# Performance work log

Hardware: AMD Instinct MI355X
Metric: run time of the kernel (lower is better)

## Reference

```python
import jax, jax.numpy as jnp
import numpy as np

N = 50000      # nodes
E = 800000     # edges (before self-loops)
IN_DIM = 256
HID = 128
HEADS = 4
HEAD_D = HID // HEADS
LAYERS = 2
EPS = 1e-5
SLOPE = 0.2    # GATv2 leaky_relu negative slope (PyG default)


def setup_inputs() -> dict:
    key = jax.random.key(0)
    ks = jax.random.split(key, 8)
    x = jax.random.normal(ks[0], (N, IN_DIM), dtype=jnp.float32)
    edge_index = jax.random.randint(ks[1], (2, E), 0, N, dtype=jnp.int64)
    s_in = (2.0 / (IN_DIM + HID)) ** 0.5
    s_h = (2.0 / (HID + HID)) ** 0.5
    return {
        'x': x,
        'W_in': jax.random.normal(ks[2], (IN_DIM, HID), dtype=jnp.float32) * s_in,
        'b_in': jnp.zeros((HID,), jnp.float32),
        'ln_in_g': jnp.ones((HID,), jnp.float32),
        'ln_in_b': jnp.zeros((HID,), jnp.float32),
        'Wl': jax.random.normal(ks[3], (LAYERS, HID, HID), dtype=jnp.float32) * s_h,
        'Wr': jax.random.normal(ks[4], (LAYERS, HID, HID), dtype=jnp.float32) * s_h,
        'att': jax.random.normal(ks[5], (LAYERS, HEADS, HEAD_D), dtype=jnp.float32) * s_h,
        'ln_g': jnp.ones((LAYERS, HID), jnp.float32),
        'ln_b': jnp.zeros((LAYERS, HID), jnp.float32),
        'edge_index': edge_index,
    }


def layer_norm(h, g, b):
    mu = jnp.mean(h, axis=-1, keepdims=True)
    var = jnp.mean(jnp.square(h - mu), axis=-1, keepdims=True)
    return (h - mu) * jax.lax.rsqrt(var + EPS) * g + b


def gatv2_conv(h, src, dst, Wl, Wr, att):
    # h: [N, HID]; src/dst: [E'] (self-loops included)
    xl = (h @ Wl).reshape(N, HEADS, HEAD_D)   # source transform (also message)
    xr = (h @ Wr).reshape(N, HEADS, HEAD_D)   # target transform
    e = jax.nn.leaky_relu(xl[src] + xr[dst], SLOPE)          # [E', H, D]
    logits = jnp.einsum('ehd,hd->eh', e, att)                # [E', H]
    # segment softmax over incoming edges of each dst node
    m = jax.lax.stop_gradient(jax.ops.segment_max(logits, dst, num_segments=N))
    a = jnp.exp(logits - m[dst])
    z = jax.ops.segment_sum(a, dst, num_segments=N)
    alpha = a / z[dst]                                       # [E', H]
    out = jax.ops.segment_sum(xl[src] * alpha[:, :, None], dst, num_segments=N)
    return out.reshape(N, HID)


def reference(x, W_in, b_in, ln_in_g, ln_in_b, Wl, Wr, att, ln_g, ln_b, edge_index):
    loops = jnp.arange(N, dtype=edge_index.dtype)
    src = jnp.concatenate([edge_index[0], loops])
    dst = jnp.concatenate([edge_index[1], loops])
    h = jax.nn.relu(layer_norm(x @ W_in + b_in, ln_in_g, ln_in_b))
    for l in range(LAYERS):
        h_new = jax.nn.elu(layer_norm(gatv2_conv(h, src, dst, Wl[l], Wr[l], att[l]), ln_g[l], ln_b[l]))
        h = h + h_new
    return h
```

## Files before the change

kernel.cpp:

```cpp
#include <hip/hip_runtime.h>
#include <hip/hip_bf16.h>


#define NN 50000
#define EE 800000
#define EP (EE + NN)
#define IN_DIM 256
#define HID 128
#define SLOPE 0.2f
#define LN_EPS 1e-5f
#define NB 196
#define L2E 1.4426950408889634f

typedef short s8v __attribute__((ext_vector_type(8)));
typedef float f4v __attribute__((ext_vector_type(4)));

__device__ __forceinline__ float u2f(unsigned int u) {
    union { unsigned int i; float f; } c; c.i = u; return c.f;
}
__device__ __forceinline__ unsigned short f2bf(float f) {
    union { float f; unsigned int i; } c; c.f = f;
    unsigned int r = (c.i + 0x7fffu + ((c.i >> 16) & 1u)) >> 16;
    return (unsigned short)r;
}
__device__ __forceinline__ void unpack8(const uint4 raw, float* m) {
    m[0] = u2f(raw.x << 16); m[1] = u2f(raw.x & 0xffff0000u);
    m[2] = u2f(raw.y << 16); m[3] = u2f(raw.y & 0xffff0000u);
    m[4] = u2f(raw.z << 16); m[5] = u2f(raw.z & 0xffff0000u);
    m[6] = u2f(raw.w << 16); m[7] = u2f(raw.w & 0xffff0000u);
}
__device__ __forceinline__ float quad_sum(float v) {
    v += __int_as_float(__builtin_amdgcn_update_dpp(
            0, __float_as_int(v), 0xB1 , 0xF, 0xF, true));
    v += __int_as_float(__builtin_amdgcn_update_dpp(
            0, __float_as_int(v), 0x4E , 0xF, 0xF, true));
    return v;
}

__global__ void prep_weights(const float* __restrict__ Win,
                             const float* __restrict__ Wl,
                             const float* __restrict__ Wr,
                             float4* __restrict__ wp) {
    const int sid = blockIdx.x * 256 + threadIdx.x;
    const float* W;
    int slot;
    if (sid < 4096) { W = Win; slot = sid; }
    else {
        const int m = (sid - 4096) >> 11;
        slot = (sid - 4096) & 2047;
        W = (m == 0) ? Wl : (m == 1) ? Wr : (m == 2) ? (Wl + 16384) : (Wr + 16384);
    }
    const int n = slot & 127;
    const int kbase = (slot >> 9) * 32 + ((slot >> 7) & 3) * 8;
    unsigned short o[8];
#pragma unroll
    for (int j = 0; j < 8; j++) o[j] = f2bf(W[(size_t)(kbase + j) * 128 + n]);
    wp[sid] = *(const float4*)o;
}

__global__ __launch_bounds__(256) void gemm_in_mfma(
        const float* __restrict__ x,
        const float4* __restrict__ wp,
        const float* __restrict__ bin,
        const float* __restrict__ g,
        const float* __restrict__ bb,
        unsigned short* __restrict__ hb) {
    __shared__ s8v wlds[4096];
    const int tid = threadIdx.x;
    const int wv = tid >> 6, lane = tid & 63;
    const int l15 = lane & 15, kseg = lane >> 4;
    const int row0 = blockIdx.x * 64 + wv * 16;
    const int arow = row0 + l15;
    const int r = (arow < NN) ? arow : 0;

    s8v afrag[8];
#pragma unroll
    for (int ks = 0; ks < 8; ks++) {
        const float* ap = x + (size_t)r * IN_DIM + ks * 32 + kseg * 8;
        const float4 a0 = *(const float4*)ap;
        const float4 a1 = *(const float4*)(ap + 4);
        unsigned short t[8] = { f2bf(a0.x), f2bf(a0.y), f2bf(a0.z), f2bf(a0.w),
                                f2bf(a1.x), f2bf(a1.y), f2bf(a1.z), f2bf(a1.w) };
        afrag[ks] = *(const s8v*)t;
    }

#pragma unroll
    for (int i = 0; i < 16; i++) {
        const int idx = i * 256 + tid;
        ((float4*)wlds)[idx] = wp[idx];
    }
    __syncthreads();

    f4v acc[8];
#pragma unroll
    for (int nb = 0; nb < 8; nb++) acc[nb] = (f4v){0.f, 0.f, 0.f, 0.f};
#pragma unroll
    for (int ks = 0; ks < 8; ks++) {
#pragma unroll
        for (int nb = 0; nb < 8; nb++) {
            const s8v bfrag = wlds[(ks * 4 + kseg) * 128 + nb * 16 + l15];
            acc[nb] = __builtin_amdgcn_mfma_f32_16x16x32_bf16(afrag[ks], bfrag, acc[nb], 0, 0, 0);
        }
    }

    float binv[8], gv[8], bbv[8];
#pragma unroll
    for (int nb = 0; nb < 8; nb++) {
        const int col = nb * 16 + l15;
        binv[nb] = bin[col]; gv[nb] = g[col]; bbv[nb] = bb[col];
    }
    float s1[4] = {0.f, 0.f, 0.f, 0.f}, s2[4] = {0.f, 0.f, 0.f, 0.f};
#pragma unroll
    for (int nb = 0; nb < 8; nb++)
#pragma unroll
        for (int reg = 0; reg < 4; reg++) {
            const float t = acc[nb][reg] + binv[nb];
            acc[nb][reg] = t;
            s1[reg] += t; s2[reg] += t * t;
        }
#pragma unroll
    for (int off = 1; off < 16; off <<= 1)
#pragma unroll
        for (int reg = 0; reg < 4; reg++) {
            s1[reg] += __shfl_xor(s1[reg], off);
            s2[reg] += __shfl_xor(s2[reg], off);
        }
    float mu[4], rstd[4];
#pragma unroll
    for (int reg = 0; reg < 4; reg++) {
        mu[reg] = s1[reg] / (float)HID;
        rstd[reg] = rsqrtf(s2[reg] / (float)HID - mu[reg] * mu[reg] + LN_EPS);
    }
    const int rbase = row0 + 4 * kseg;
#pragma unroll
    for (int reg = 0; reg < 4; reg++) {
        const int grow = rbase + reg;
        if (grow >= NN) continue;
#pragma unroll
        for (int nb = 0; nb < 8; nb++) {
            const int col = nb * 16 + l15;
            float v = (acc[nb][reg] - mu[reg]) * rstd[reg] * gv[nb] + bbv[nb];
            hb[(size_t)grow * HID + col] = f2bf(fmaxf(v, 0.f));
        }
    }
}

__global__ __launch_bounds__(256) void gemm_xlxr_mfma(
        const unsigned short* __restrict__ hb,
        const float4* __restrict__ wp,
        unsigned short* __restrict__ xl,
        unsigned short* __restrict__ xrb) {
    __shared__ s8v wlds[4096];
    const int tid = threadIdx.x;
    const int wv = tid >> 6, lane = tid & 63;
    const int l15 = lane & 15, kseg = lane >> 4;
    const int row0 = blockIdx.x * 64 + wv * 16;
    const int arow = row0 + l15;
    const int r = (arow < NN) ? arow : 0;

    s8v afrag[4];
#pragma unroll
    for (int ks = 0; ks < 4; ks++)
        afrag[ks] = *(const s8v*)(hb + (size_t)r * HID + ks * 32 + kseg * 8);

#pragma unroll
    for (int i = 0; i < 16; i++) {
        const int idx = i * 256 + tid;
        ((float4*)wlds)[idx] = wp[idx];
    }
    __syncthreads();

    f4v accL[8], accR[8];
#pragma unroll
    for (int nb = 0; nb < 8; nb++) {
        accL[nb] = (f4v){0.f, 0.f, 0.f, 0.f};
        accR[nb] = (f4v){0.f, 0.f, 0.f, 0.f};
    }
#pragma unroll
    for (int ks = 0; ks < 4; ks++) {
#pragma unroll
        for (int nb = 0; nb < 8; nb++) {
            const s8v bL = wlds[(ks * 4 + kseg) * 128 + nb * 16 + l15];
            accL[nb] = __builtin_amdgcn_mfma_f32_16x16x32_bf16(afrag[ks], bL, accL[nb], 0, 0, 0);
            const s8v bR = wlds[2048 + (ks * 4 + kseg) * 128 + nb * 16 + l15];
            accR[nb] = __builtin_amdgcn_mfma_f32_16x16x32_bf16(afrag[ks], bR, accR[nb], 0, 0, 0);
        }
    }

    const int rbase = row0 + 4 * kseg;
#pragma unroll
    for (int reg = 0; reg < 4; reg++) {
        const int grow = rbase + reg;
        if (grow >= NN) continue;
#pragma unroll
        for (int nb = 0; nb < 8; nb++) {
            const int col = nb * 16 + l15;
            xl[(size_t)grow * HID + col]  = f2bf(accL[nb][reg]);
            xrb[(size_t)grow * HID + col] = f2bf(accR[nb][reg]);
        }
    }
}

__global__ void dst_hist(const int* __restrict__ ei, int* __restrict__ cnt,
                         unsigned short* __restrict__ epos) {
    const long e = (long)blockIdx.x * 256 + threadIdx.x;
    if (e >= EP) return;
    const int d = (e < EE) ? ei[EE + e] : (int)(e - EE);
    epos[e] = (unsigned short)atomicAdd(&cnt[d], 1);
}

__global__ void scan_bsum(const int* __restrict__ cnt, int* __restrict__ bsum) {
    const int tid = threadIdx.x;
    const int i = blockIdx.x * 256 + tid;
    int v = (i < NN) ? cnt[i] : 0;
#pragma unroll
    for (int off = 1; off < 64; off <<= 1) v += __shfl_xor(v, off);
    __shared__ int ws[4];
    if ((tid & 63) == 0) ws[tid >> 6] = v;
    __syncthreads();
    if (tid == 0) bsum[blockIdx.x] = ws[0] + ws[1] + ws[2] + ws[3];
}

__global__ void scan_bpre(const int* __restrict__ bsum, int* __restrict__ bpre) {
    const int t = threadIdx.x;
    const int lane = t & 63, wv = t >> 6;
    const int v = (t < NB) ? bsum[t] : 0;
    int s = v;
#pragma unroll
    for (int off = 1; off < 64; off <<= 1) {
        const int u = __shfl_up(s, off);
        if (lane >= off) s += u;
    }
    __shared__ int wt[4];
    if (lane == 63) wt[wv] = s;
    __syncthreads();
    int add = 0;
    for (int w = 0; w < wv; w++) add += wt[w];
    if (t < NB) bpre[t] = s + add - v;
}

__global__ void scan_rowptr(const int* __restrict__ cnt,
                            const int* __restrict__ bpre,
                            int* __restrict__ rowptr) {
    const int tid = threadIdx.x;
    const int lane = tid & 63, wv = tid >> 6;
    const int i = blockIdx.x * 256 + tid;
    const int v = (i < NN) ? cnt[i] : 0;
    int s = v;
#pragma unroll
    for (int off = 1; off < 64; off <<= 1) {
        const int u = __shfl_up(s, off);
        if (lane >= off) s += u;
    }
    __shared__ int wt[4];
    if (lane == 63) wt[wv] = s;
    __syncthreads();
    int add = bpre[blockIdx.x];
    for (int w = 0; w < wv; w++) add += wt[w];
    const int excl = s + add - v;
    if (i < NN) rowptr[i] = excl;
    if (i == NN - 1) rowptr[NN] = excl + v;
}

__global__ void csr_scatter(const int* __restrict__ ei,
                            const int* __restrict__ rowptr,
                            const unsigned short* __restrict__ epos,
                            unsigned short* __restrict__ esrc16) {
    const long e = (long)blockIdx.x * 256 + threadIdx.x;
    if (e >= EP) return;
    int s, d;
    if (e < EE) { s = ei[e]; d = ei[EE + e]; }
    else        { s = d = (int)(e - EE); }
    esrc16[rowptr[d] + epos[e]] = (unsigned short)s;
}

__global__ __launch_bounds__(256) void gat_ln(
        const unsigned short* __restrict__ xl,
        const unsigned short* __restrict__ xrb,
        const float* __restrict__ att,
        const int* __restrict__ rowptr,
        const unsigned short* __restrict__ esrc16,
        const float* __restrict__ g,
        const float* __restrict__ b,
        const unsigned short* __restrict__ hres,
        float* __restrict__ dest,
        unsigned short* __restrict__ destb) {
    const int tid = threadIdx.x;
    const int lane = tid & 63;
    const int wv = tid >> 6;
    const int l16 = lane & 15;
    const int grp = lane >> 4;
    const int node = blockIdx.x * 16 + wv * 4 + grp;
    const int f0 = l16 * 8;

    float xrv[8], a06[8], a04[8];
    {
        const uint4 xraw = *(const uint4*)(xrb + (size_t)node * HID + f0);
        unpack8(xraw, xrv);
        const float4 t0 = *(const float4*)(att + f0);
        const float4 t1 = *(const float4*)(att + f0 + 4);
        float av[8] = { t0.x, t0.y, t0.z, t0.w, t1.x, t1.y, t1.z, t1.w };
#pragma unroll
        for (int j = 0; j < 8; j++) {
            a06[j] = 0.6f * L2E * av[j];
            a04[j] = 0.4f * L2E * av[j];
        }
    }
    const int beg = rowptr[node];
    const int deg = rowptr[node + 1] - beg;
    int dmax = deg;
    dmax = max(dmax, __shfl_xor(dmax, 16));
    dmax = max(dmax, __shfl_xor(dmax, 32));

    const char* xlbase = (const char*)xl + f0 * 2;
    const int gb = lane & 48;

    float acc[8];
#pragma unroll
    for (int j = 0; j < 8; j++) acc[j] = 0.f;
    float z = 0.f;

    int sb = (l16 < deg) ? (int)esrc16[beg + l16] : 0;

#define PROCR(RAW, VALID) do {                                              \
        float m[8];                                                         \
        unpack8((RAW), m);                                                  \
        float v = 0.f;                                                      \
        _Pragma("unroll")                                                   \
        for (int j = 0; j < 8; j++) {                                       \
            const float tt = m[j] + xrv[j];                                 \
            v += tt * a06[j] + fabsf(tt) * a04[j];                          \
        }                                                                   \
        v = quad_sum(v);                           \
        const float a = (VALID) ? __builtin_amdgcn_exp2f(v) : 0.f;          \
        z += a;                                                             \
        _Pragma("unroll")                                                   \
        for (int j = 0; j < 8; j++) acc[j] = fmaf(a, m[j], acc[j]);         \
    } while (0)

    for (int t = 0; t < dmax; t += 8) {
        if ((t & 15) == 0 && t) {
            sb = (t + l16 < deg) ? (int)esrc16[beg + t + l16] : 0;
        }
        int o[8];
#pragma unroll
        for (int i = 0; i < 8; i++)
            o[i] = __shfl(sb, gb | ((t + i) & 15)) << 8;
        uint4 r[8];
#pragma unroll
        for (int i = 0; i < 8; i++)
            r[i] = *(const uint4*)(xlbase + o[i]);
#pragma unroll
        for (int i = 0; i < 8; i++)
            PROCR(r[i], t + i < deg);
    }
#undef PROCR

    const float inv = 1.f / z;
    float o[8];
    float s1 = 0.f, s2 = 0.f;
#pragma unroll
    for (int j = 0; j < 8; j++) {
        o[j] = acc[j] * inv;
        s1 += o[j];
        s2 = fmaf(o[j], o[j], s2);
    }
#pragma unroll
    for (int off = 1; off < 16; off <<= 1) {
        s1 += __shfl_xor(s1, off);
        s2 += __shfl_xor(s2, off);
    }
    const float mu = s1 / (float)HID;
    const float rstd = rsqrtf(s2 / (float)HID - mu * mu + LN_EPS);

    float gv[8], bv[8], hv[8];
    {
        const float4 g0 = *(const float4*)(g + f0);
        const float4 g1 = *(const float4*)(g + f0 + 4);
        gv[0]=g0.x; gv[1]=g0.y; gv[2]=g0.z; gv[3]=g0.w;
        gv[4]=g1.x; gv[5]=g1.y; gv[6]=g1.z; gv[7]=g1.w;
        const float4 b0 = *(const float4*)(b + f0);
        const float4 b1 = *(const float4*)(b + f0 + 4);
        bv[0]=b0.x; bv[1]=b0.y; bv[2]=b0.z; bv[3]=b0.w;
        bv[4]=b1.x; bv[5]=b1.y; bv[6]=b1.z; bv[7]=b1.w;
        const uint4 hraw = *(const uint4*)(hres + (size_t)node * HID + f0);
        unpack8(hraw, hv);
    }
    float res[8];
#pragma unroll
    for (int j = 0; j < 8; j++) {
        float n = (o[j] - mu) * rstd * gv[j] + bv[j];
        n = (n > 0.f) ? n : (__builtin_amdgcn_exp2f(n * L2E) - 1.f);
        res[j] = hv[j] + n;
    }
    if (dest) {
        float* dp = dest + (size_t)node * HID + f0;
        *(float4*)dp       = (float4){res[0], res[1], res[2], res[3]};
        *(float4*)(dp + 4) = (float4){res[4], res[5], res[6], res[7]};
    }
    if (destb) {
        unsigned short o16[8];
#pragma unroll
        for (int j = 0; j < 8; j++) o16[j] = f2bf(res[j]);
        *(uint4*)(destb + (size_t)node * HID + f0) = *(const uint4*)o16;
    }
}

extern "C" void kernel_launch(void* const* d_in, const int* in_sizes, int n_in,
                              void* d_out, int out_size, void* d_ws, size_t ws_size,
                              hipStream_t stream) {
    const float* x       = (const float*)d_in[0];
    const float* W_in    = (const float*)d_in[1];
    const float* b_in    = (const float*)d_in[2];
    const float* ln_in_g = (const float*)d_in[3];
    const float* ln_in_b = (const float*)d_in[4];
    const float* Wl      = (const float*)d_in[5];
    const float* Wr      = (const float*)d_in[6];
    const float* att     = (const float*)d_in[7];
    const float* ln_g    = (const float*)d_in[8];
    const float* ln_b    = (const float*)d_in[9];
    const int*   ei      = (const int*)d_in[10];
    float* out = (float*)d_out;

    unsigned short* hb  = (unsigned short*)d_ws;
    unsigned short* hb2 = hb  + (size_t)NN * HID;
    unsigned short* xlb = hb2 + (size_t)NN * HID;
    unsigned short* xrb = xlb + (size_t)NN * HID;
    float4* wp = (float4*)(xrb + (size_t)NN * HID);
    int* cnt    = (int*)(wp + 12288);
    int* rowptr = cnt + NN;
    int* bsum   = rowptr + (NN + 1);
    int* bpre   = bsum + NB;
    unsigned short* epos   = (unsigned short*)(bpre + NB);
    unsigned short* esrc16 = epos + EP;

    prep_weights<<<48, 256, 0, stream>>>(W_in, Wl, Wr, wp);

    (void)hipMemsetAsync(cnt, 0, NN * sizeof(int), stream);
    const int eblocks = (EP + 255) / 256;
    dst_hist<<<eblocks, 256, 0, stream>>>(ei, cnt, epos);
    scan_bsum<<<NB, 256, 0, stream>>>(cnt, bsum);
    scan_bpre<<<1, 256, 0, stream>>>(bsum, bpre);
    scan_rowptr<<<NB, 256, 0, stream>>>(cnt, bpre, rowptr);
    csr_scatter<<<eblocks, 256, 0, stream>>>(ei, rowptr, epos, esrc16);

    const int mblocks = (NN + 63) / 64;
    gemm_in_mfma<<<mblocks, 256, 0, stream>>>(x, wp, b_in, ln_in_g, ln_in_b, hb);

    for (int l = 0; l < 2; l++) {
        const unsigned short* hsrc = (l == 0) ? hb : hb2;
        gemm_xlxr_mfma<<<mblocks, 256, 0, stream>>>(hsrc, wp + 4096 + l * 4096, xlb, xrb);
        gat_ln<<<NN / 16, 256, 0, stream>>>(xlb, xrb, att + (size_t)l * HID,
                                            rowptr, esrc16,
                                            ln_g + (size_t)l * HID,
                                            ln_b + (size_t)l * HID,
                                            hsrc,
                                            (l == 1) ? out : (float*)nullptr,
                                            (l == 0) ? hb2 : (unsigned short*)nullptr);
    }
}
```

Before: 189.3 us.

## Assign one wavefront per node, splitting edges across four lane groups

The GAT aggregation kernel now maps one 64-lane wavefront to each destination node instead of packing four nodes per wavefront. The four 16-lane groups each process a different edge, with partial accumulators and softmax denominators combined by cross-group shuffles, and only group 0 writes the LayerNorm result. This is meant to remove the load imbalance of padding each wavefront to the largest degree among its four nodes. The cost is fewer independent loads in flight per lane (one gather per iteration instead of eight batched), extra reduction shuffles, and four times as many blocks.

```diff
diff --git a/kernel.cpp b/kernel.cpp
--- a/kernel.cpp
+++ b/kernel.cpp
@@ -290,7 +290,7 @@
     const int wv = tid >> 6;
     const int l16 = lane & 15;
     const int grp = lane >> 4;
-    const int node = blockIdx.x * 16 + wv * 4 + grp;
+    const int node = blockIdx.x * 4 + wv;
     const int f0 = l16 * 8;
 
     float xrv[8], a06[8], a04[8];
@@ -308,19 +308,15 @@
     }
     const int beg = rowptr[node];
     const int deg = rowptr[node + 1] - beg;
-    int dmax = deg;
-    dmax = max(dmax, __shfl_xor(dmax, 16));
-    dmax = max(dmax, __shfl_xor(dmax, 32));
 
     const char* xlbase = (const char*)xl + f0 * 2;
-    const int gb = lane & 48;
 
     float acc[8];
 #pragma unroll
     for (int j = 0; j < 8; j++) acc[j] = 0.f;
     float z = 0.f;
 
-    int sb = (l16 < deg) ? (int)esrc16[beg + l16] : 0;
+    int sb = (lane < deg) ? (int)esrc16[beg + lane] : 0;
 
 #define PROCR(RAW, VALID) do {                                              \
         float m[8];                                                         \
@@ -338,23 +334,24 @@
         for (int j = 0; j < 8; j++) acc[j] = fmaf(a, m[j], acc[j]);         \
     } while (0)
 
-    for (int t = 0; t < dmax; t += 8) {
-        if ((t & 15) == 0 && t) {
-            sb = (t + l16 < deg) ? (int)esrc16[beg + t + l16] : 0;
-        }
-        int o[8];
-#pragma unroll
-        for (int i = 0; i < 8; i++)
-            o[i] = __shfl(sb, gb | ((t + i) & 15)) << 8;
-        uint4 r[8];
-#pragma unroll
-        for (int i = 0; i < 8; i++)
-            r[i] = *(const uint4*)(xlbase + o[i]);
-#pragma unroll
-        for (int i = 0; i < 8; i++)
-            PROCR(r[i], t + i < deg);
+    for (int t = 0; t < deg; t += 4) {
+        if ((t & 63) == 0 && t) {
+            sb = (t + lane < deg) ? (int)esrc16[beg + t + lane] : 0;
+        }
+        const int e = t + grp;
+        const int off = __shfl(sb, e & 63) << 8;
+        const uint4 raw = *(const uint4*)(xlbase + off);
+        PROCR(raw, e < deg);
     }
 #undef PROCR
+
+#pragma unroll
+    for (int j = 0; j < 8; j++) {
+        acc[j] += __shfl_xor(acc[j], 16);
+        acc[j] += __shfl_xor(acc[j], 32);
+    }
+    z += __shfl_xor(z, 16);
+    z += __shfl_xor(z, 32);
 
     const float inv = 1.f / z;
     float o[8];
@@ -373,36 +370,38 @@
     const float mu = s1 / (float)HID;
     const float rstd = rsqrtf(s2 / (float)HID - mu * mu + LN_EPS);
 
-    float gv[8], bv[8], hv[8];
-    {
-        const float4 g0 = *(const float4*)(g + f0);
-        const float4 g1 = *(const float4*)(g + f0 + 4);
-        gv[0]=g0.x; gv[1]=g0.y; gv[2]=g0.z; gv[3]=g0.w;
-        gv[4]=g1.x; gv[5]=g1.y; gv[6]=g1.z; gv[7]=g1.w;
-        const float4 b0 = *(const float4*)(b + f0);
-        const float4 b1 = *(const float4*)(b + f0 + 4);
-        bv[0]=b0.x; bv[1]=b0.y; bv[2]=b0.z; bv[3]=b0.w;
-        bv[4]=b1.x; bv[5]=b1.y; bv[6]=b1.z; bv[7]=b1.w;
-        const uint4 hraw = *(const uint4*)(hres + (size_t)node * HID + f0);
-        unpack8(hraw, hv);
-    }
-    float res[8];
-#pragma unroll
-    for (int j = 0; j < 8; j++) {
-        float n = (o[j] - mu) * rstd * gv[j] + bv[j];
-        n = (n > 0.f) ? n : (__builtin_amdgcn_exp2f(n * L2E) - 1.f);
-        res[j] = hv[j] + n;
-    }
-    if (dest) {
-        float* dp = dest + (size_t)node * HID + f0;
-        *(float4*)dp       = (float4){res[0], res[1], res[2], res[3]};
-        *(float4*)(dp + 4) = (float4){res[4], res[5], res[6], res[7]};
-    }
-    if (destb) {
-        unsigned short o16[8];
-#pragma unroll
-        for (int j = 0; j < 8; j++) o16[j] = f2bf(res[j]);
-        *(uint4*)(destb + (size_t)node * HID + f0) = *(const uint4*)o16;
+    if (grp == 0) {
+        float gv[8], bv[8], hv[8];
+        {
+            const float4 g0 = *(const float4*)(g + f0);
+            const float4 g1 = *(const float4*)(g + f0 + 4);
+            gv[0]=g0.x; gv[1]=g0.y; gv[2]=g0.z; gv[3]=g0.w;
+            gv[4]=g1.x; gv[5]=g1.y; gv[6]=g1.z; gv[7]=g1.w;
+            const float4 b0 = *(const float4*)(b + f0);
+            const float4 b1 = *(const float4*)(b + f0 + 4);
+            bv[0]=b0.x; bv[1]=b0.y; bv[2]=b0.z; bv[3]=b0.w;
+            bv[4]=b1.x; bv[5]=b1.y; bv[6]=b1.z; bv[7]=b1.w;
+            const uint4 hraw = *(const uint4*)(hres + (size_t)node * HID + f0);
+            unpack8(hraw, hv);
+        }
+        float res[8];
+#pragma unroll
+        for (int j = 0; j < 8; j++) {
+            float n = (o[j] - mu) * rstd * gv[j] + bv[j];
+            n = (n > 0.f) ? n : (__builtin_amdgcn_exp2f(n * L2E) - 1.f);
+            res[j] = hv[j] + n;
+        }
+        if (dest) {
+            float* dp = dest + (size_t)node * HID + f0;
+            *(float4*)dp       = (float4){res[0], res[1], res[2], res[3]};
+            *(float4*)(dp + 4) = (float4){res[4], res[5], res[6], res[7]};
+        }
+        if (destb) {
+            unsigned short o16[8];
+#pragma unroll
+            for (int j = 0; j < 8; j++) o16[j] = f2bf(res[j]);
+            *(uint4*)(destb + (size_t)node * HID + f0) = *(const uint4*)o16;
+        }
     }
 }
 
@@ -450,12 +449,12 @@
     for (int l = 0; l < 2; l++) {
         const unsigned short* hsrc = (l == 0) ? hb : hb2;
         gemm_xlxr_mfma<<<mblocks, 256, 0, stream>>>(hsrc, wp + 4096 + l * 4096, xlb, xrb);
-        gat_ln<<<NN / 16, 256, 0, stream>>>(xlb, xrb, att + (size_t)l * HID,
-                                            rowptr, esrc16,
-                                            ln_g + (size_t)l * HID,
-                                            ln_b + (size_t)l * HID,
-                                            hsrc,
-                                            (l == 1) ? out : (float*)nullptr,
-                                            (l == 0) ? hb2 : (unsigned short*)nullptr);
-    }
-}
+        gat_ln<<<NN / 4, 256, 0, stream>>>(xlb, xrb, att + (size_t)l * HID,
+                                           rowptr, esrc16,
+                                           ln_g + (size_t)l * HID,
+                                           ln_b + (size_t)l * HID,
+                                           hsrc,
+                                           (l == 1) ? out : (float*)nullptr,
+                                           (l == 0) ? hb2 : (unsigned short*)nullptr);
+    }
+}
```

Measured after the change: 197.5 us. 4.3% more time.
